# Optimization experiments

Measured on AMD Instinct MI355X. Metric: run time of the kernel, lower is better.

The kernel has to match this reference:

```python
import jax, jax.numpy as jnp
import numpy as np

K_SIZE, STRIDE, PAD = 3, 2, 1

def _conv1x1(x, w, b):
    return jnp.einsum('bchw,oc->bohw', x, w) + b[None, :, None, None]

def _unfold(x, k, s, p):
    # Matches torch F.unfold ordering: channel-major, then (kh, kw). -> [B, C, k*k, L]
    B, C, H, W = x.shape
    xp = jnp.pad(x, ((0, 0), (0, 0), (p, p), (p, p)))
    ho = (H + 2 * p - k) // s + 1
    wo = (W + 2 * p - k) // s + 1
    cols = []
    for i in range(k):
        for j in range(k):
            cols.append(xp[:, :, i:i + s * (ho - 1) + 1:s, j:j + s * (wo - 1) + 1:s])
    patches = jnp.stack(cols, axis=2)            # [B, C, k*k, ho, wo]
    return patches.reshape(B, C, k * k, ho * wo)

def _forward(shallow, deep, K_w, K_b, KSA_w, KSA_b):
    B, C, H, W = shallow.shape
    d = (2 * C) // 16
    h, w = H // STRIDE, W // STRIDE
    hw = h * w
    max_out = _conv1x1(deep, KSA_w, KSA_b)            # [B, d, h, w]
    # global re-score branch
    max_out1 = jnp.max(max_out, axis=1)               # [B, h, w]
    q = max_out1.reshape(B, hw)                       # [B, hw]
    kt = max_out.reshape(B, hw, d)                    # faithful to torch .view(B,-1,d) (channel-scrambled flat view)
    lit = jnp.einsum('bp,bpd->bd', q, kt) / hw        # mean over hw of outer products -> [B, d]
    V = max_out.reshape(B, d, hw)
    re_score = jnp.einsum('bd,bdp->bp', lit, V).reshape(B, 1, h, w)
    sig = jax.nn.sigmoid(re_score)
    # local windowed attention branch
    Kx = _conv1x1(shallow, K_w, K_b)                  # [B, out, H, W]
    Kunf = _unfold(Kx, K_SIZE, STRIDE, PAD)           # [B, out, kk, hw]
    # torch does matmul([d,1],[1,kk]) then mean over d == mean_d(q_d) * K patch element
    qmean = jnp.mean(max_out, axis=1).reshape(B, 1, 1, hw)
    logits = qmean * Kunf                             # [B, out, kk, hw]
    new_kernel = jax.nn.softmax(logits, axis=2)       # softmax over window dim kk
    att = jnp.sum(new_kernel * Kunf, axis=2)          # [B, out, hw]
    att = att.reshape(B, -1, h, w)
    return sig * att + att, re_score

def setup_inputs():
    key = jax.random.key(0)
    ks = jax.random.split(key, 6)
    B, C, H, W = 4, 256, 128, 128
    out_c, d = 256, (2 * C) // 16
    return {
        'shallow': jax.random.normal(ks[0], (B, C, H, W), jnp.float32),
        'deep': jax.random.normal(ks[1], (B, 2 * C, H // 2, W // 2), jnp.float32),
        'K_w': jax.random.normal(ks[2], (out_c, C), jnp.float32) * 0.02,
        'K_b': jax.random.normal(ks[3], (out_c,), jnp.float32) * 0.02,
        'KSA_w': jax.random.normal(ks[4], (d, 2 * C), jnp.float32) * 0.02,
        'KSA_b': jax.random.normal(ks[5], (d,), jnp.float32) * 0.02,
    }

def reference(shallow, deep, K_w, K_b, KSA_w, KSA_b):
    return _forward(shallow, deep, K_w, K_b, KSA_w, KSA_b)
```

## Files before the change

kernel.cpp:

```cpp
#include <hip/hip_runtime.h>

typedef unsigned short u16;
typedef __attribute__((ext_vector_type(8))) short short8;
typedef __attribute__((ext_vector_type(4))) float float4v;
typedef __attribute__((ext_vector_type(4))) unsigned short ushort4v;

__device__ __forceinline__ u16 f2bf(float f) {
    unsigned u = __float_as_uint(f);
    u += 0x7FFFu + ((u >> 16) & 1u);
    return (u16)(u >> 16);
}
__device__ __forceinline__ float bf2f(u16 u) {
    return __uint_as_float(((unsigned)u) << 16);
}

__device__ __forceinline__ void lds_barrier() {
    asm volatile("s_waitcnt lgkmcnt(0)\n\ts_barrier" ::: "memory");
}

__device__ float g_maxout[4 * 32 * 4096];
__device__ float g_q[16384];
__device__ float g_qmean[16384];
__device__ float g_lit[128];
__device__ float g_sigfac[16384];
__device__ u16   g_KwP[65536];
__device__ u16   g_KSAwP[16384];
__device__ u16   g_Kx[4 * 256 * 16384];

__global__ __launch_bounds__(256) void prep_kernel(
    const float* __restrict__ Kw, const float* __restrict__ KSAw)
{
    const int idx = blockIdx.x * 256 + threadIdx.x;
    if (idx < 128) g_lit[idx] = 0.f;
    if (idx < 65536) {
        const int o = idx >> 8, c = idx & 255;
        const int fi = ((o >> 4) << 3) + (c >> 5);
        const int ln = (((c >> 3) & 3) << 4) + (o & 15);
        g_KwP[fi * 512 + ln * 8 + (c & 7)] = f2bf(Kw[idx]);
    }
    if (idx < 16384) {
        const int o = idx >> 9, c = idx & 511;
        const int fi = ((c >> 5) << 1) + (o >> 4);
        const int ln = (((c >> 3) & 3) << 4) + (o & 15);
        g_KSAwP[fi * 512 + ln * 8 + (c & 7)] = f2bf(KSAw[idx]);
    }
}

__global__ __launch_bounds__(256) void gemm_deep(
    const float* __restrict__ Bias, const float* __restrict__ X)
{
    __shared__ u16 As[16384];
    const int t = threadIdx.x;
    const int wave = t >> 6, lane = t & 63;
    const int quad = lane >> 4, n16 = lane & 15;
    const int b = blockIdx.y;
    const int p = blockIdx.x * 64 + wave * 16 + n16;
    const float* Xb = X + ((long long)b << 21) + p;

#pragma unroll
    for (int i = 0; i < 8; i++)
        *(short8*)(As + ((i << 8) + t) * 8) = *(const short8*)(g_KSAwP + ((i << 8) + t) * 8);

    float xr[3][8];
#define DXLOAD(dst, kb_) { \
    const float* xp_ = Xb + ((((kb_) << 5) + (quad << 3)) << 12); \
    _Pragma("unroll") for (int j = 0; j < 8; j++) dst[j] = xp_[j << 12]; }

    DXLOAD(xr[0], 0)
    DXLOAD(xr[1], 1)
    DXLOAD(xr[2], 2)

    __syncthreads();

    float4v acc[2];
#pragma unroll
    for (int i = 0; i < 2; i++) acc[i] = (float4v){0.f, 0.f, 0.f, 0.f};

#pragma unroll
    for (int kb = 0; kb < 16; kb++) {
        short8 bfrag;
#pragma unroll
        for (int j = 0; j < 8; j++) bfrag[j] = (short)f2bf(xr[kb % 3][j]);
        if (kb < 13) DXLOAD(xr[(kb + 3) % 3], kb + 3)
#pragma unroll
        for (int ot = 0; ot < 2; ot++) {
            const short8 afrag = *(const short8*)(As + (((kb << 1) + ot) << 9) + lane * 8);
            acc[ot] = __builtin_amdgcn_mfma_f32_16x16x32_bf16(afrag, bfrag, acc[ot], 0, 0, 0);
        }
    }
#undef DXLOAD

    float mx = -3.4e38f, sm = 0.f;
#pragma unroll
    for (int ot = 0; ot < 2; ot++) {
#pragma unroll
        for (int r = 0; r < 4; r++) {
            const int o = ot * 16 + quad * 4 + r;
            const float v = acc[ot][r] + Bias[o];
            g_maxout[((b * 32 + o) << 12) + p] = v;
            mx = fmaxf(mx, v);
            sm += v;
        }
    }
    mx = fmaxf(mx, __shfl_xor(mx, 16, 64));
    sm += __shfl_xor(sm, 16, 64);
    mx = fmaxf(mx, __shfl_xor(mx, 32, 64));
    sm += __shfl_xor(sm, 32, 64);
    if (quad == 0) {
        g_q[(b << 12) + p] = mx;
        g_qmean[(b << 12) + p] = sm * (1.f / 32.f);
    }
}

__global__ __launch_bounds__(256) void lit_kernel()
{
    const int b = blockIdx.y;
    const int f0 = blockIdx.x * 8192;
    const int t = threadIdx.x;
    const float* mo = g_maxout + (b << 17);
    const float* qb = g_q + (b << 12);
    float acc = 0.f;
#pragma unroll
    for (int it = 0; it < 32; it++) {
        const int f = f0 + it * 256 + t;
        acc += qb[f >> 5] * mo[f];
    }
    __shared__ float red[256];
    red[t] = acc;
    __syncthreads();
    if (t < 32) {
        float s = 0.f;
#pragma unroll
        for (int k = 0; k < 8; k++) s += red[t + k * 32];
        atomicAdd(&g_lit[b * 32 + t], s * (1.f / 4096.f));
    }
}

__global__ __launch_bounds__(256) void rescore_kernel(float* __restrict__ out_re)
{
    const int idx = blockIdx.x * 256 + threadIdx.x;
    const int b = idx >> 12, p = idx & 4095;
    const float* mo = g_maxout + (b << 17) + p;
    const float* lb = g_lit + b * 32;
    float r = 0.f;
#pragma unroll
    for (int j = 0; j < 32; j++) r += lb[j] * mo[j << 12];
    out_re[idx] = r;
    g_sigfac[idx] = 1.f + 1.f / (1.f + __expf(-r));
}

__global__ __launch_bounds__(256) void gemm_kx(
    const float* __restrict__ Bias, const float* __restrict__ X)
{
    __shared__ u16 As[2][8192];
    const int t = threadIdx.x;
    const int wave = t >> 6, lane = t & 63;
    const int quad = lane >> 4, n16 = lane & 15;
    const int b = blockIdx.y;
    const int p0 = blockIdx.x * 64;
    const float* Xb = X + ((long long)b << 22) + p0 + wave * 16 + n16;

    const u16* agbase = g_KwP + wave * 16384 + lane * 8;
    const int alds = wave * 2048 + lane * 8;

    float xr[3][8];
#define XLOAD(dst, kb_) { \
    const float* xp_ = Xb + ((((kb_) << 5) + (quad << 3)) << 14); \
    _Pragma("unroll") for (int j = 0; j < 8; j++) dst[j] = xp_[j << 14]; }

    float4v acc[16];
#pragma unroll
    for (int i = 0; i < 16; i++) acc[i] = (float4v){0.f, 0.f, 0.f, 0.f};

    {
        short8 areg[4];
#pragma unroll
        for (int i = 0; i < 4; i++) areg[i] = *(const short8*)(agbase + i * 4096);
        XLOAD(xr[0], 0)
        XLOAD(xr[1], 1)
        XLOAD(xr[2], 2)
#pragma unroll
        for (int i = 0; i < 4; i++) *(short8*)(&As[0][alds + i * 512]) = areg[i];
    }
    lds_barrier();

#pragma unroll
    for (int kb = 0; kb < 8; kb++) {
        short8 areg[4];
        if (kb < 7) {
#pragma unroll
            for (int i = 0; i < 4; i++)
                areg[i] = *(const short8*)(agbase + i * 4096 + (kb + 1) * 512);
        }
        short8 bfrag;
#pragma unroll
        for (int j = 0; j < 8; j++) bfrag[j] = (short)f2bf(xr[kb % 3][j]);
        if (kb < 5) XLOAD(xr[(kb + 3) % 3], kb + 3)

        const u16* ap = &As[kb & 1][lane * 8];
#pragma unroll
        for (int ot = 0; ot < 16; ot++) {
            const short8 afrag = *(const short8*)(ap + ot * 512);
            acc[ot] = __builtin_amdgcn_mfma_f32_16x16x32_bf16(
                bfrag, afrag, acc[ot], 0, 0, 0);
        }

        if (kb < 7) {
#pragma unroll
            for (int i = 0; i < 4; i++)
                *(short8*)(&As[(kb + 1) & 1][alds + i * 512]) = areg[i];
            lds_barrier();
        }
    }
#undef XLOAD

    u16* kxb = g_Kx + (((long long)b << 8) << 14);
#pragma unroll
    for (int ot = 0; ot < 16; ot++) {
        const int o = ot * 16 + n16;
        const float bo = Bias[o];
        ushort4v w;
#pragma unroll
        for (int r = 0; r < 4; r++) w[r] = f2bf(acc[ot][r] + bo);
        *(ushort4v*)(kxb + ((long long)o << 14) + p0 + wave * 16 + (quad << 2)) = w;
    }
}

__global__ __launch_bounds__(256) void att_window(float* __restrict__ out)
{
    __shared__ float tile[8][9][130];
    const int t = threadIdx.x;
    const int o0 = blockIdx.y << 3, b = blockIdx.z;
    const int y0 = (blockIdx.x << 3) - 1;
    const u16* kxb = g_Kx + (((long long)b << 8) << 14);

    if (t < 72) tile[t / 9][t % 9][64] = 0.f;
#pragma unroll
    for (int k = 0; k < 18; k++) {
        const int e = (k << 8) + t;
        const int row = e >> 6, pr = e & 63;
        const int oi = row / 9, r = row - oi * 9;
        const int y = y0 + r;
        unsigned v = 0;
        if (y >= 0 && y < 128)
            v = *(const unsigned*)(kxb + (((long long)(o0 + oi)) << 14) + (y << 7) + (pr << 1));
        tile[oi][r][pr] = bf2f((u16)(v & 0xffffu));
        tile[oi][r][65 + pr] = bf2f((u16)(v >> 16));
    }
    __syncthreads();

    const int p = (blockIdx.x << 8) + t;
    const int pw = t & 63;
    const int rl = (t >> 6) << 1;
    const float m = g_qmean[(b << 12) + p];
    const float sf = g_sigfac[(b << 12) + p];

#pragma unroll
    for (int oi = 0; oi < 8; oi++) {
        float v[9];
#pragma unroll
        for (int ki = 0; ki < 3; ++ki) {
            v[ki * 3 + 0] = tile[oi][rl + ki][64 + pw];
            v[ki * 3 + 1] = tile[oi][rl + ki][pw];
            v[ki * 3 + 2] = tile[oi][rl + ki][65 + pw];
        }
        float mx = -3.4e38f;
#pragma unroll
        for (int k = 0; k < 9; ++k) mx = fmaxf(mx, m * v[k]);
        float s = 0.f, a = 0.f;
#pragma unroll
        for (int k = 0; k < 9; ++k) {
            const float e = __expf(m * v[k] - mx);
            s += e;
            a += e * v[k];
        }
        out[((((long long)b << 8) + o0 + oi) << 12) + p] = (a / s) * sf;
    }
}

extern "C" void kernel_launch(void* const* d_in, const int* in_sizes, int n_in,
                              void* d_out, int out_size, void* d_ws, size_t ws_size,
                              hipStream_t stream) {
    const float *shallow = 0, *deep = 0, *K_w = 0, *K_b = 0, *KSA_w = 0, *KSA_b = 0;
    for (int i = 0; i < n_in; ++i) {
        switch (in_sizes[i]) {
            case 16777216: shallow = (const float*)d_in[i]; break;
            case 8388608:  deep    = (const float*)d_in[i]; break;
            case 65536:    K_w     = (const float*)d_in[i]; break;
            case 256:      K_b     = (const float*)d_in[i]; break;
            case 16384:    KSA_w   = (const float*)d_in[i]; break;
            case 32:       KSA_b   = (const float*)d_in[i]; break;
        }
    }
    float* out = (float*)d_out;

    prep_kernel<<<320, 256, 0, stream>>>(K_w, KSA_w);
    gemm_deep<<<dim3(64, 4), 256, 0, stream>>>(KSA_b, deep);
    lit_kernel<<<dim3(16, 4), 256, 0, stream>>>();
    rescore_kernel<<<64, 256, 0, stream>>>(out + 4194304);
    gemm_kx<<<dim3(256, 4), 256, 0, stream>>>(K_b, shallow);
    att_window<<<dim3(16, 32, 4), 256, 0, stream>>>(out);
}
```

Measured before the change: 181.7 us.

## Add transposed maxout copy, widen lit grid, store att_window tile as bf16

gemm_deep now also writes a pixel-major transposed copy of max_out, so rescore_kernel can read 32 contiguous floats per pixel with vector loads instead of strided column reads. It runs with 128 blocks of 128 threads. lit_kernel is spread over 8x more blocks, each doing fewer iterations, which raises parallelism in this small reduction at the cost of more atomics. att_window keeps its LDS tile as bf16 rather than float, halving shared-memory footprint to allow more resident blocks, and converts to float on each read. The extra transposed write adds global traffic in gemm_deep.

```diff
diff --git a/kernel.cpp b/kernel.cpp
--- a/kernel.cpp
+++ b/kernel.cpp
@@ -19,6 +19,7 @@
 }
 
 __device__ float g_maxout[4 * 32 * 4096];
+__device__ float g_maxoutT[4 * 4096 * 32];
 __device__ float g_q[16384];
 __device__ float g_qmean[16384];
 __device__ float g_lit[128];
@@ -93,14 +94,16 @@
     float mx = -3.4e38f, sm = 0.f;
 #pragma unroll
     for (int ot = 0; ot < 2; ot++) {
+        float4v vv;
 #pragma unroll
         for (int r = 0; r < 4; r++) {
             const int o = ot * 16 + quad * 4 + r;
-            const float v = acc[ot][r] + Bias[o];
-            g_maxout[((b * 32 + o) << 12) + p] = v;
-            mx = fmaxf(mx, v);
-            sm += v;
-        }
+            vv[r] = acc[ot][r] + Bias[o];
+            g_maxout[((b * 32 + o) << 12) + p] = vv[r];
+            mx = fmaxf(mx, vv[r]);
+            sm += vv[r];
+        }
+        *(float4v*)(g_maxoutT + (((b << 12) + p) << 5) + ot * 16 + quad * 4) = vv;
     }
     mx = fmaxf(mx, __shfl_xor(mx, 16, 64));
     sm += __shfl_xor(sm, 16, 64);
@@ -115,13 +118,13 @@
 __global__ __launch_bounds__(256) void lit_kernel()
 {
     const int b = blockIdx.y;
-    const int f0 = blockIdx.x * 8192;
+    const int f0 = blockIdx.x * 1024;
     const int t = threadIdx.x;
     const float* mo = g_maxout + (b << 17);
     const float* qb = g_q + (b << 12);
     float acc = 0.f;
 #pragma unroll
-    for (int it = 0; it < 32; it++) {
+    for (int it = 0; it < 4; it++) {
         const int f = f0 + it * 256 + t;
         acc += qb[f >> 5] * mo[f];
     }
@@ -136,15 +139,19 @@
     }
 }
 
-__global__ __launch_bounds__(256) void rescore_kernel(float* __restrict__ out_re)
-{
-    const int idx = blockIdx.x * 256 + threadIdx.x;
-    const int b = idx >> 12, p = idx & 4095;
-    const float* mo = g_maxout + (b << 17) + p;
-    const float* lb = g_lit + b * 32;
+__global__ __launch_bounds__(128) void rescore_kernel(float* __restrict__ out_re)
+{
+    const int idx = blockIdx.x * 128 + threadIdx.x;
+    const int b = idx >> 12;
+    const float4v* mt = (const float4v*)(g_maxoutT + (idx << 5));
+    const float4v* lb = (const float4v*)(g_lit + b * 32);
     float r = 0.f;
 #pragma unroll
-    for (int j = 0; j < 32; j++) r += lb[j] * mo[j << 12];
+    for (int j = 0; j < 8; j++) {
+        const float4v m4 = mt[j];
+        const float4v l4 = lb[j];
+        r += m4[0] * l4[0] + m4[1] * l4[1] + m4[2] * l4[2] + m4[3] * l4[3];
+    }
     out_re[idx] = r;
     g_sigfac[idx] = 1.f + 1.f / (1.f + __expf(-r));
 }
@@ -228,13 +235,13 @@
 
 __global__ __launch_bounds__(256) void att_window(float* __restrict__ out)
 {
-    __shared__ float tile[8][9][130];
+    __shared__ u16 tile[8][9][132];
     const int t = threadIdx.x;
     const int o0 = blockIdx.y << 3, b = blockIdx.z;
     const int y0 = (blockIdx.x << 3) - 1;
     const u16* kxb = g_Kx + (((long long)b << 8) << 14);
 
-    if (t < 72) tile[t / 9][t % 9][64] = 0.f;
+    if (t < 72) tile[t / 9][t % 9][64] = 0;
 #pragma unroll
     for (int k = 0; k < 18; k++) {
         const int e = (k << 8) + t;
@@ -244,8 +251,8 @@
         unsigned v = 0;
         if (y >= 0 && y < 128)
             v = *(const unsigned*)(kxb + (((long long)(o0 + oi)) << 14) + (y << 7) + (pr << 1));
-        tile[oi][r][pr] = bf2f((u16)(v & 0xffffu));
-        tile[oi][r][65 + pr] = bf2f((u16)(v >> 16));
+        tile[oi][r][pr] = (u16)(v & 0xffffu);
+        tile[oi][r][65 + pr] = (u16)(v >> 16);
     }
     __syncthreads();
 
@@ -260,9 +267,9 @@
         float v[9];
 #pragma unroll
         for (int ki = 0; ki < 3; ++ki) {
-            v[ki * 3 + 0] = tile[oi][rl + ki][64 + pw];
-            v[ki * 3 + 1] = tile[oi][rl + ki][pw];
-            v[ki * 3 + 2] = tile[oi][rl + ki][65 + pw];
+            v[ki * 3 + 0] = bf2f(tile[oi][rl + ki][64 + pw]);
+            v[ki * 3 + 1] = bf2f(tile[oi][rl + ki][pw]);
+            v[ki * 3 + 2] = bf2f(tile[oi][rl + ki][65 + pw]);
         }
         float mx = -3.4e38f;
 #pragma unroll
@@ -296,8 +303,8 @@
 
     prep_kernel<<<320, 256, 0, stream>>>(K_w, KSA_w);
     gemm_deep<<<dim3(64, 4), 256, 0, stream>>>(KSA_b, deep);
-    lit_kernel<<<dim3(16, 4), 256, 0, stream>>>();
-    rescore_kernel<<<64, 256, 0, stream>>>(out + 4194304);
+    lit_kernel<<<dim3(128, 4), 256, 0, stream>>>();
+    rescore_kernel<<<128, 128, 0, stream>>>(out + 4194304);
     gemm_kx<<<dim3(256, 4), 256, 0, stream>>>(K_b, shallow);
     att_window<<<dim3(16, 32, 4), 256, 0, stream>>>(out);
 }
```

New measurement: 181.6 us. About the same (-0.1%).
